# Kernel optimization log

Measured on AMD Instinct MI355X. Metric: run time of the kernel, lower is better.

## Reference

```python
import jax, jax.numpy as jnp
import numpy as np


def dct_matrix(n):
    # orthonormal DCT-II matrix, matches scipy.fftpack.dct(norm='ortho')
    k = jnp.arange(n, dtype=jnp.float32)[:, None]
    i = jnp.arange(n, dtype=jnp.float32)[None, :]
    D = jnp.cos(jnp.pi * (2.0 * i + 1.0) * k / (2.0 * n))
    s = jnp.where(k == 0, jnp.sqrt(1.0 / n), jnp.sqrt(2.0 / n))
    return (D * s).astype(jnp.float32)


def mad_mask(h, w):
    eps = 1e-10
    v1 = int(min(h, w) * 0.1)
    v2 = int(min(h, w) * 0.7)
    v3 = min(h, w)
    xy = jnp.maximum(jnp.arange(h, dtype=jnp.float32)[:, None],
                     jnp.arange(w, dtype=jnp.float32)[None, :])
    m = jnp.where(xy <= v1, 1.0 - xy / (v1 + eps) * 0.95,
        jnp.where(xy <= v2, 0.01,
        jnp.where(xy <= v3, (xy - v2) / (v3 - v2) * 0.3, 0.5)))
    return m.astype(jnp.float32)


def setup_inputs() -> dict:
    key = jax.random.key(0)
    ks = jax.random.split(key, 8)
    num_layers, token_length, C = 24, 100, 1024
    N, B = 1024, 32  # h = w = 32
    patch = 16
    val = np.sqrt(6.0 / float(3 * patch * patch + C))
    feats = jax.random.normal(ks[0], (1 + N, B, C), dtype=jnp.float32)
    learnable_tokens = jax.random.uniform(ks[1], (num_layers, token_length, C),
                                          minval=-val, maxval=val, dtype=jnp.float32)
    lim = 1.0 / np.sqrt(C)
    W_t2f = jax.random.uniform(ks[2], (C, C), minval=-lim, maxval=lim, dtype=jnp.float32)
    b_t2f = jax.random.uniform(ks[3], (C,), minval=-lim, maxval=lim, dtype=jnp.float32)
    W_df = jax.random.uniform(ks[4], (C, C), minval=-lim, maxval=lim, dtype=jnp.float32)
    b_df = jax.random.uniform(ks[5], (C,), minval=-lim, maxval=lim, dtype=jnp.float32)
    return {
        'feats': feats,
        'layer': 5,
        'learnable_tokens': learnable_tokens,
        'scale': jnp.float32(0.001),
        'W_t2f': W_t2f,
        'b_t2f': b_t2f,
        'W_df': W_df,
        'b_df': b_df,
    }


def reference(feats, layer, learnable_tokens, scale, W_t2f, b_t2f, W_df, b_df):
    # has_cls_token=True, batch_first=False (defaults)
    cls_tok, x = feats[:1], feats[1:]          # [1,B,C], [N,B,C]
    N, B, C = x.shape
    h = int(np.sqrt(N)); w = h
    # NOTE: original does a raw reshape (N,B,C) -> (B,C,h,w); replicate faithfully.
    ximg = x.reshape(B, C, h, w)
    # --- MAD_decompose: 2D orthonormal DCT-II per (b, c) image ---
    D = dct_matrix(h)
    feat_dct = jnp.einsum('ik,bckl,jl->bcij', D, ximg, D)
    mask = mad_mask(h, w)                      # [h,w]
    cal = feat_dct * (1.0 - mask)              # high-frequency (causal) part
    cal = cal.reshape(N, B, C)                 # raw reshape as in torch code
    # --- forward_delta_feat ---
    tokens = learnable_tokens[layer]           # [M,C]
    attn = jnp.einsum('nbc,mc->nbm', cal, tokens) * (C ** -0.5)
    attn = jax.nn.softmax(attn, axis=-1)
    t2f = tokens[1:] @ W_t2f.T + b_t2f         # [M-1,C]
    df = jnp.einsum('nbm,mc->nbc', attn[:, :, 1:], t2f)
    df = (df + cal) @ W_df.T + b_df            # [N,B,C]
    # --- MAD_compose_fast: ifft2 approximation of IDCT, clamp to [0,255] ---
    fc = df.reshape(B, C, h, w).astype(jnp.complex64)
    out = jnp.clip(jnp.real(jnp.fft.ifft2(fc, norm='ortho')), 0.0, 255.0)
    out = out.reshape(N, B, C).astype(jnp.float32)
    x = x + out * scale
    return jnp.concatenate([cls_tok, x], axis=0)
```

## Files before the change

kernel.cpp:

```cpp
#include <hip/hip_runtime.h>

typedef unsigned short u16;
typedef u16 ushort8 __attribute__((ext_vector_type(8)));
typedef u16 ushort4v __attribute__((ext_vector_type(4)));
typedef __bf16 bf16x8 __attribute__((ext_vector_type(8)));
typedef float f32x4 __attribute__((ext_vector_type(4)));

#define PI_F 3.14159265358979323846f

__device__ __forceinline__ u16 f2bf(float f) {
  union { float f; unsigned int u; } v; v.f = f;
  unsigned int r = v.u + 0x7fffu + ((v.u >> 16) & 1u);
  return (u16)(r >> 16);
}
__device__ __forceinline__ float bf2f(u16 u) {
  union { unsigned int u; float f; } v; v.u = ((unsigned int)u) << 16;
  return v.f;
}

__device__ __forceinline__ void gload16(const u16* g, u16* l) {
  __builtin_amdgcn_global_load_lds((const __attribute__((address_space(1))) void*)g,
                                   (__attribute__((address_space(3))) void*)l, 16, 0, 0);
}

__device__ __forceinline__ void stage_tile(const u16* __restrict__ G, int ld, int row0, int k0,
                                           u16* lds, int wid, int lane) {
  int seg = wid * 32;
  const u16* gp = G + (size_t)(row0 + seg + (lane >> 2)) * ld + k0 + (lane & 3) * 8;
  gload16(gp, lds + seg * 32);
  gload16(gp + (size_t)16 * ld, lds + (seg + 16) * 32);
}

#define WAIT_VM(N) asm volatile("s_waitcnt vmcnt(" #N ")" ::: "memory")
#define RAW_BARRIER() asm volatile("s_barrier" ::: "memory")

__device__ __forceinline__ float im_val(int r, int c) {
  float xy = (float)(r > c ? r : c);
  float m = (xy <= 3.0f) ? (1.0f - xy * (0.95f / 3.0f))
           : ((xy <= 22.0f) ? 0.01f : ((xy - 22.0f) * 0.03f));
  return 1.0f - m;
}
__device__ __forceinline__ float dct_val(int r, int c) {
  int a = ((2 * c + 1) * r) & 127;
  float s = (r == 0) ? 0.17677669529663687f : 0.25f;
  return cosf((float)a * (PI_F / 64.0f)) * s;
}

__global__ __launch_bounds__(256) void k_prep(const float* __restrict__ feats,
                                              const float* __restrict__ lt, const int* __restrict__ layerp,
                                              const float* __restrict__ Wt2f,
                                              u16* __restrict__ xb, u16* __restrict__ wt_bf,
                                              u16* __restrict__ tok_bf, u16* __restrict__ A2,
                                              float* __restrict__ outp) {
  int tid = blockIdx.x * 256 + threadIdx.x;
  int L = *layerp;
  const float4* in4 = (const float4*)(feats + 32768);
  ushort4v* xb4 = (ushort4v*)xb;
  #pragma unroll
  for (int rep = 0; rep < 16; ++rep) {
    int j = tid + rep * 524288;
    float4 v = in4[j];
    ushort4v o;
    o[0] = f2bf(v.x); o[1] = f2bf(v.y); o[2] = f2bf(v.z); o[3] = f2bf(v.w);
    xb4[j] = o;
  }
  ((ushort8*)A2)[tid] = (ushort8){0,0,0,0,0,0,0,0};
  if (tid < 262144) {
    float4 v = ((const float4*)Wt2f)[tid];
    ushort4v o;
    o[0] = f2bf(v.x); o[1] = f2bf(v.y); o[2] = f2bf(v.z); o[3] = f2bf(v.w);
    ((ushort4v*)wt_bf)[tid] = o;
  }
  if (tid < 32768) {
    outp[tid] = feats[tid];
    int m = tid >> 8;
    ushort4v o = (ushort4v){0,0,0,0};
    if (m < 99) {
      float4 v = *(const float4*)(lt + (size_t)L * 102400 + (size_t)(m + 1) * 1024 + (tid & 255) * 4);
      o[0] = f2bf(v.x); o[1] = f2bf(v.y); o[2] = f2bf(v.z); o[3] = f2bf(v.w);
    }
    ((ushort4v*)tok_bf)[tid] = o;
  }
}

__device__ void mdct_row(const float* __restrict__ row, u16* __restrict__ dst, float* sm, int t) {
  float* Ms = sm; float* T1 = sm + 1056; float* Dsh = sm + 2112;
  for (int i = t; i < 1024; i += 256) {
    int r = i >> 5, c = i & 31;
    Dsh[r * 33 + c] = dct_val(r, c);
    Ms[r * 33 + c] = row[i] * im_val(r, c);
  }
  __syncthreads();
  int k = t >> 3, l0 = (t & 7) * 4;
  float a0 = 0, a1 = 0, a2 = 0, a3 = 0;
  #pragma unroll 8
  for (int i = 0; i < 32; ++i) {
    float d = Dsh[i * 33 + k];
    const float* mr = &Ms[i * 33 + l0];
    a0 += d * mr[0]; a1 += d * mr[1]; a2 += d * mr[2]; a3 += d * mr[3];
  }
  T1[k * 33 + l0 + 0] = a0; T1[k * 33 + l0 + 1] = a1;
  T1[k * 33 + l0 + 2] = a2; T1[k * 33 + l0 + 3] = a3;
  __syncthreads();
  float b0 = 0, b1 = 0, b2 = 0, b3 = 0;
  #pragma unroll 8
  for (int j = 0; j < 32; ++j) {
    float u = T1[k * 33 + j];
    b0 += u * Dsh[j * 33 + l0 + 0];
    b1 += u * Dsh[j * 33 + l0 + 1];
    b2 += u * Dsh[j * 33 + l0 + 2];
    b3 += u * Dsh[j * 33 + l0 + 3];
  }
  ushort4v o;
  o[0] = f2bf(b0); o[1] = f2bf(b1); o[2] = f2bf(b2); o[3] = f2bf(b3);
  *(ushort4v*)(dst + k * 32 + l0) = o;
}

__global__ __launch_bounds__(256) void k_setupA(const float* __restrict__ Wdf, const float* __restrict__ bdf,
                                                const float* __restrict__ lt, const int* __restrict__ layerp,
                                                float* __restrict__ weff_f, u16* __restrict__ weff_bf,
                                                float* __restrict__ beff, u16* __restrict__ tok2) {
  __shared__ __align__(16) float sm[14784];
  int bid = blockIdx.x, t = threadIdx.x;
  if (bid < 256) {
    float* In = sm; float* Uc = sm + 4224; float* Us = sm + 8448;
    float* Csh = sm + 12672; float* Ssh = sm + 13728;
    int c0 = bid * 4;
    for (int i = t; i < 1024; i += 256) {
      int r = i >> 5, c = i & 31;
      float ang = (float)((r * c) & 31) * (PI_F / 16.0f);
      Csh[r * 33 + c] = cosf(ang); Ssh[r * 33 + c] = sinf(ang);
    }
    { int cc = t & 3, v0 = t >> 2;
      for (int v = v0; v < 1024; v += 64)
        In[cc * 1056 + (v >> 5) * 33 + (v & 31)] = Wdf[(size_t)v * 1024 + c0 + cc]; }
    __syncthreads();
    int cc = t >> 6, L2 = t & 63, p = L2 & 31, h = L2 >> 5;
    for (int j = h * 16; j < h * 16 + 16; ++j) {
      float ac = 0, as = 0;
      #pragma unroll 8
      for (int i = 0; i < 32; ++i) {
        float m = In[cc * 1056 + i * 33 + j];
        ac += Csh[p * 33 + i] * m;
        as += Ssh[p * 33 + i] * m;
      }
      Uc[cc * 1056 + p * 33 + j] = ac;
      Us[cc * 1056 + p * 33 + j] = as;
    }
    __syncthreads();
    for (int q = h * 16; q < h * 16 + 16; ++q) {
      float acc = 0;
      #pragma unroll 8
      for (int j = 0; j < 32; ++j)
        acc += Uc[cc * 1056 + p * 33 + j] * Csh[q * 33 + j] -
               Us[cc * 1056 + p * 33 + j] * Ssh[q * 33 + j];
      float val = acc * 0.03125f;
      size_t idx = (size_t)(p * 32 + q) * 1024 + c0 + cc;
      weff_f[idx] = val;
      weff_bf[idx] = f2bf(val);
    }
  } else if (bid == 256) {
    float* Bsh = sm; float* Uc = sm + 1056; float* Us = sm + 2112;
    float* Csh = sm + 3168; float* Ssh = sm + 4224;
    for (int i = t; i < 1024; i += 256) {
      int r = i >> 5, c = i & 31;
      float ang = (float)((r * c) & 31) * (PI_F / 16.0f);
      Csh[r * 33 + c] = cosf(ang); Ssh[r * 33 + c] = sinf(ang);
      Bsh[r * 33 + c] = bdf[i];
    }
    __syncthreads();
    for (int idx = t; idx < 1024; idx += 256) {
      int p = idx >> 5, j = idx & 31;
      float ac = 0, as = 0;
      #pragma unroll 8
      for (int i = 0; i < 32; ++i) {
        float m = Bsh[i * 33 + j];
        ac += Csh[p * 33 + i] * m;
        as += Ssh[p * 33 + i] * m;
      }
      Uc[p * 33 + j] = ac; Us[p * 33 + j] = as;
    }
    __syncthreads();
    for (int idx = t; idx < 1024; idx += 256) {
      int p = idx >> 5, q = idx & 31;
      float acc = 0;
      #pragma unroll 8
      for (int jj = 0; jj < 32; ++jj)
        acc += Uc[p * 33 + jj] * Csh[q * 33 + jj] - Us[p * 33 + jj] * Ssh[q * 33 + jj];
      beff[idx] = acc * 0.03125f;
    }
  } else {
    int p = bid - 257;
    if (p >= 100) {
      *(ushort4v*)(tok2 + (size_t)p * 1024 + t * 4) = (ushort4v){0,0,0,0};
      return;
    }
    mdct_row(lt + (size_t)(*layerp) * 102400 + (size_t)p * 1024, tok2 + (size_t)p * 1024, sm, t);
  }
}

template <int NT>
__device__ __forceinline__ void gemm128_core(const u16* __restrict__ A, int lda,
                                             const u16* __restrict__ B, int ldb,
                                             int g0, int c0, u16* smem,
                                             f32x4 (&acc)[4][4], int wid, int lane) {
  int wr = wid >> 1, wc = wid & 1, cl = lane & 15, rg = lane >> 4;
  stage_tile(A, lda, g0, 0, smem, wid, lane);
  stage_tile(B, ldb, c0, 0, smem + 12288, wid, lane);
  stage_tile(A, lda, g0, 32, smem + 4096, wid, lane);
  stage_tile(B, ldb, c0, 32, smem + 16384, wid, lane);
  int cur = 0;
  #pragma unroll 1
  for (int kt = 0; kt < NT; ++kt) {
    if (kt == NT - 1) { WAIT_VM(0); } else { WAIT_VM(4); }
    RAW_BARRIER();
    if (kt + 2 < NT) {
      int slot = (cur == 0) ? 2 : cur - 1;
      stage_tile(A, lda, g0, (kt + 2) * 32, smem + slot * 4096, wid, lane);
      stage_tile(B, ldb, c0, (kt + 2) * 32, smem + 12288 + slot * 4096, wid, lane);
    }
    const u16* pa = smem + cur * 4096;
    const u16* pb = smem + 12288 + cur * 4096;
    bf16x8 af[4], bv[4];
    #pragma unroll
    for (int mf = 0; mf < 4; mf++)
      af[mf] = *(const bf16x8*)(pa + (wr * 64 + mf * 16 + cl) * 32 + rg * 8);
    #pragma unroll
    for (int nf = 0; nf < 4; nf++)
      bv[nf] = *(const bf16x8*)(pb + (wc * 64 + nf * 16 + cl) * 32 + rg * 8);
    #pragma unroll
    for (int mf = 0; mf < 4; mf++)
      #pragma unroll
      for (int nf = 0; nf < 4; nf++)
        acc[mf][nf] = __builtin_amdgcn_mfma_f32_16x16x32_bf16(af[mf], bv[nf], acc[mf][nf], 0, 0, 0);
    cur = (cur == 2) ? 0 : cur + 1;
  }
}

__global__ __launch_bounds__(256) void k_setupB(const float* __restrict__ weff_f,
                                                const u16* __restrict__ tok_bf, const u16* __restrict__ wt_bf,
                                                const float* __restrict__ bt2f,
                                                u16* __restrict__ w2, u16* __restrict__ t2f) {
  __shared__ __align__(16) u16 smem[24576];
  int bid = blockIdx.x, t = threadIdx.x;
  if (bid < 1024) {
    mdct_row(weff_f + (size_t)bid * 1024, w2 + (size_t)bid * 1024, (float*)smem, t);
  } else {
    int bn = bid - 1024;
    int lane = t & 63, wid = t >> 6;
    int wr = wid >> 1, wc = wid & 1, cl = lane & 15, rg = lane >> 4;
    f32x4 acc[4][4];
    #pragma unroll
    for (int i = 0; i < 4; i++)
      #pragma unroll
      for (int j = 0; j < 4; j++) acc[i][j] = (f32x4){0.f,0.f,0.f,0.f};
    gemm128_core<32>(tok_bf, 1024, wt_bf, 1024, 0, bn * 128, smem, acc, wid, lane);
    #pragma unroll
    for (int mf = 0; mf < 4; mf++)
      #pragma unroll
      for (int nf = 0; nf < 4; nf++) {
        int col = bn * 128 + wc * 64 + nf * 16 + cl;
        #pragma unroll
        for (int r = 0; r < 4; r++) {
          int row = wr * 64 + mf * 16 + rg * 4 + r;
          t2f[(size_t)row * 1024 + col] = (row < 99) ? f2bf(acc[mf][nf][r] + bt2f[col]) : (u16)0;
        }
      }
  }
}

__global__ __launch_bounds__(256) void k_setupC(const u16* __restrict__ weff_bf, const u16* __restrict__ t2f,
                                                const u16* __restrict__ xb, const u16* __restrict__ tok2,
                                                u16* __restrict__ Gt, u16* __restrict__ A2) {
  __shared__ __align__(16) u16 smem[24576];
  int bid = blockIdx.x, t = threadIdx.x;
  int lane = t & 63, wid = t >> 6;
  if (bid < 8) {
    int wr = wid >> 1, wc = wid & 1, cl = lane & 15, rg = lane >> 4;
    f32x4 acc[4][4];
    #pragma unroll
    for (int i = 0; i < 4; i++)
      #pragma unroll
      for (int j = 0; j < 4; j++) acc[i][j] = (f32x4){0.f,0.f,0.f,0.f};
    gemm128_core<32>(weff_bf, 1024, t2f, 1024, bid * 128, 0, smem, acc, wid, lane);
    #pragma unroll
    for (int mf = 0; mf < 4; mf++)
      #pragma unroll
      for (int nf = 0; nf < 4; nf++) {
        int col = wc * 64 + nf * 16 + cl;
        #pragma unroll
        for (int r = 0; r < 4; r++) {
          int row = bid * 128 + wr * 64 + mf * 16 + rg * 4 + r;
          Gt[(size_t)row * 128 + col] = f2bf(acc[mf][nf][r]);
        }
      }
  } else {
    int g0 = (bid - 8) * 128;
    int cl = lane & 15, rg = lane >> 4;
    f32x4 acc[2][7];
    #pragma unroll
    for (int i = 0; i < 2; i++)
      #pragma unroll
      for (int j = 0; j < 7; j++) acc[i][j] = (f32x4){0.f,0.f,0.f,0.f};
    stage_tile(xb, 1024, g0, 0, smem, wid, lane);
    stage_tile(tok2, 1024, 0, 0, smem + 12288, wid, lane);
    stage_tile(xb, 1024, g0, 32, smem + 4096, wid, lane);
    stage_tile(tok2, 1024, 0, 32, smem + 16384, wid, lane);
    int cur = 0;
    #pragma unroll 1
    for (int kt = 0; kt < 32; ++kt) {
      if (kt == 31) { WAIT_VM(0); } else { WAIT_VM(4); }
      RAW_BARRIER();
      if (kt + 2 < 32) {
        int slot = (cur == 0) ? 2 : cur - 1;
        stage_tile(xb, 1024, g0, (kt + 2) * 32, smem + slot * 4096, wid, lane);
        stage_tile(tok2, 1024, 0, (kt + 2) * 32, smem + 12288 + slot * 4096, wid, lane);
      }
      const u16* pa = smem + cur * 4096;
      const u16* pb = smem + 12288 + cur * 4096;
      bf16x8 a0 = *(const bf16x8*)(pa + (wid * 32 + cl) * 32 + rg * 8);
      bf16x8 a1 = *(const bf16x8*)(pa + (wid * 32 + 16 + cl) * 32 + rg * 8);
      #pragma unroll
      for (int nf = 0; nf < 7; nf++) {
        bf16x8 bv = *(const bf16x8*)(pb + (nf * 16 + cl) * 32 + rg * 8);
        acc[0][nf] = __builtin_amdgcn_mfma_f32_16x16x32_bf16(a0, bv, acc[0][nf], 0, 0, 0);
        acc[1][nf] = __builtin_amdgcn_mfma_f32_16x16x32_bf16(a1, bv, acc[1][nf], 0, 0, 0);
      }
      cur = (cur == 2) ? 0 : cur + 1;
    }
    #pragma unroll
    for (int mf = 0; mf < 2; mf++) {
      #pragma unroll
      for (int r = 0; r < 4; r++) {
        int grow = g0 + wid * 32 + mf * 16 + rg * 4 + r;
        float v[7];
        float mx = -1e30f;
        #pragma unroll
        for (int nf = 0; nf < 7; nf++) {
          int m = nf * 16 + cl;
          v[nf] = acc[mf][nf][r] * 0.03125f;
          if (m < 100) mx = fmaxf(mx, v[nf]);
        }
        #pragma unroll
        for (int d = 1; d < 16; d <<= 1) mx = fmaxf(mx, __shfl_xor(mx, d));
        float s = 0;
        #pragma unroll
        for (int nf = 0; nf < 7; nf++) {
          int m = nf * 16 + cl;
          float e = (m < 100) ? __expf(v[nf] - mx) : 0.0f;
          v[nf] = e; s += e;
        }
        #pragma unroll
        for (int d = 1; d < 16; d <<= 1) s += __shfl_xor(s, d);
        float inv = 1.0f / s;
        #pragma unroll
        for (int nf = 0; nf < 7; nf++) {
          int m = nf * 16 + cl;
          if (m >= 1 && m < 100) A2[(size_t)grow * 128 + (m - 1)] = f2bf(v[nf] * inv);
        }
      }
    }
  }
}

__global__ __launch_bounds__(256) void k_main(const u16* __restrict__ xb, const u16* __restrict__ w2,
                                              const u16* __restrict__ a2, const u16* __restrict__ gt,
                                              const float* __restrict__ beff, const float* __restrict__ feats,
                                              const float* __restrict__ scalep, float* __restrict__ outf) {
  __shared__ __align__(16) u16 smem[24576];
  int t = threadIdx.x, lane = t & 63, wid = t >> 6;
  int bid = blockIdx.x;
  int xcd = bid & 7, local = bid >> 3;
  int super = local >> 5, within = local & 31;
  int bm = xcd * 32 + super * 4 + (within & 3);
  int bn = within >> 2;
  int g0 = bm * 128, c0 = bn * 128;
  int wr = wid >> 1, wc = wid & 1;
  int cl = lane & 15, rg = lane >> 4;
  f32x4 acc[4][4];
  #pragma unroll
  for (int i = 0; i < 4; i++)
    #pragma unroll
    for (int j = 0; j < 4; j++) acc[i][j] = (f32x4){0.f,0.f,0.f,0.f};

  auto stage = [&](int kt, int slot) {
    u16* sa = smem + slot * 4096;
    u16* sb = smem + 12288 + slot * 4096;
    if (kt < 32) {
      stage_tile(xb, 1024, g0, kt * 32, sa, wid, lane);
      stage_tile(w2, 1024, c0, kt * 32, sb, wid, lane);
    } else {
      int k0 = (kt - 32) * 32;
      stage_tile(a2, 128, g0, k0, sa, wid, lane);
      stage_tile(gt, 128, c0, k0, sb, wid, lane);
    }
  };

  stage(0, 0);
  stage(1, 1);
  int cur = 0;
  #pragma unroll 1
  for (int kt = 0; kt < 36; ++kt) {
    if (kt == 35) { WAIT_VM(0); } else { WAIT_VM(4); }
    RAW_BARRIER();
    if (kt + 2 < 36) stage(kt + 2, (cur == 0) ? 2 : cur - 1);
    const u16* pa = smem + cur * 4096;
    const u16* pb = smem + 12288 + cur * 4096;
    bf16x8 af[4], bv[4];
    #pragma unroll
    for (int mf = 0; mf < 4; mf++)
      af[mf] = *(const bf16x8*)(pa + (wr * 64 + mf * 16 + cl) * 32 + rg * 8);
    #pragma unroll
    for (int nf = 0; nf < 4; nf++)
      bv[nf] = *(const bf16x8*)(pb + (wc * 64 + nf * 16 + cl) * 32 + rg * 8);
    #pragma unroll
    for (int mf = 0; mf < 4; mf++)
      #pragma unroll
      for (int nf = 0; nf < 4; nf++)
        acc[mf][nf] = __builtin_amdgcn_mfma_f32_16x16x32_bf16(af[mf], bv[nf], acc[mf][nf], 0, 0, 0);
    cur = (cur == 2) ? 0 : cur + 1;
  }

  float sc = *scalep;
  #pragma unroll
  for (int mf = 0; mf < 4; mf++) {
    #pragma unroll
    for (int nf = 0; nf < 4; nf++) {
      int col = c0 + wc * 64 + nf * 16 + cl;
      #pragma unroll
      for (int r = 0; r < 4; r++) {
        int row = g0 + wr * 64 + mf * 16 + rg * 4 + r;
        size_t idx = (size_t)row * 1024 + col;
        float val = acc[mf][nf][r] + beff[col];
        float rr = fminf(fmaxf(val, 0.f), 255.f);
        outf[32768 + idx] = feats[32768 + idx] + rr * sc;
      }
    }
  }
}

extern "C" void kernel_launch(void* const* d_in, const int* in_sizes, int n_in,
                              void* d_out, int out_size, void* d_ws, size_t ws_size,
                              hipStream_t stream) {
  const float* feats  = (const float*)d_in[0];
  const int*   layerp = (const int*)d_in[1];
  const float* lt     = (const float*)d_in[2];
  const float* scalep = (const float*)d_in[3];
  const float* Wt2f   = (const float*)d_in[4];
  const float* bt2f   = (const float*)d_in[5];
  const float* Wdf    = (const float*)d_in[6];
  const float* bdf    = (const float*)d_in[7];
  float* outp = (float*)d_out;

  char* ws = (char*)d_ws;
  float* beff   = (float*)(ws + 0);
  float* weff_f = (float*)(ws + 65536);
  u16* weff_bf = (u16*)(ws + 4259840);
  u16* w2      = (u16*)(ws + 6356992);
  u16* tok_bf  = (u16*)(ws + 8454144);
  u16* wt_bf   = (u16*)(ws + 8716288);
  u16* tok2    = (u16*)(ws + 10813440);
  u16* t2f     = (u16*)(ws + 11075584);
  u16* Gt      = (u16*)(ws + 11337728);
  u16* A2      = (u16*)(ws + 11599872);
  u16* xb      = (u16*)(ws + 19988480);

  k_prep<<<2048, 256, 0, stream>>>(feats, lt, layerp, Wt2f, xb, wt_bf, tok_bf, A2, outp);
  k_setupA<<<385, 256, 0, stream>>>(Wdf, bdf, lt, layerp, weff_f, weff_bf, beff, tok2);
  k_setupB<<<1032, 256, 0, stream>>>(weff_f, tok_bf, wt_bf, bt2f, w2, t2f);
  k_setupC<<<264, 256, 0, stream>>>(weff_bf, t2f, xb, tok2, Gt, A2);
  k_main<<<2048, 256, 0, stream>>>(xb, w2, A2, Gt, beff, feats, scalep, outp);
}
```

Measured before the change: 246.8 us.

## Enlarge main GEMM tile to 256x256 with swizzled LDS and split-K staging

The main fused GEMM kernel moves from 128x128 tiles with 4 waves to 256x256 tiles with 8 waves per block, each wave owning a 128x64 output patch. LDS staging now uses an XOR swizzle to avoid bank conflicts, and a 64-wide K step is split into two 32-wide halves with separate barriers so loads for upcoming halves overlap with compute. MFMA issue priority is raised around the matrix-multiply bursts. The larger tile cuts global and L2 traffic per FLOP, at the cost of 128KB LDS per block and higher register pressure, and the grid drops to 512 blocks.

```diff
diff --git a/kernel.cpp b/kernel.cpp
--- a/kernel.cpp
+++ b/kernel.cpp
@@ -32,6 +32,7 @@
 }
 
 #define WAIT_VM(N) asm volatile("s_waitcnt vmcnt(" #N ")" ::: "memory")
+#define WAIT_LGKM0() asm volatile("s_waitcnt lgkmcnt(0)" ::: "memory")
 #define RAW_BARRIER() asm volatile("s_barrier" ::: "memory")
 
 __device__ __forceinline__ float im_val(int r, int c) {
@@ -363,77 +364,106 @@
   }
 }
 
-__global__ __launch_bounds__(256) void k_main(const u16* __restrict__ xb, const u16* __restrict__ w2,
-                                              const u16* __restrict__ a2, const u16* __restrict__ gt,
-                                              const float* __restrict__ beff, const float* __restrict__ feats,
-                                              const float* __restrict__ scalep, float* __restrict__ outf) {
-  __shared__ __align__(16) u16 smem[24576];
-  int t = threadIdx.x, lane = t & 63, wid = t >> 6;
+__global__ __launch_bounds__(512, 2) void k_main(const u16* __restrict__ xb, const u16* __restrict__ w2,
+                                                 const u16* __restrict__ a2, const u16* __restrict__ gt,
+                                                 const float* __restrict__ beff, const float* __restrict__ feats,
+                                                 const float* __restrict__ scalep, float* __restrict__ outf) {
+  __shared__ __align__(16) u16 smem[65536];
+  int tid = threadIdx.x, lane = tid & 63, wid = tid >> 6;
+  int wr = wid >> 2, wc = wid & 3;
+  int cl = lane & 15, rg = lane >> 4;
   int bid = blockIdx.x;
-  int xcd = bid & 7, local = bid >> 3;
-  int super = local >> 5, within = local & 31;
-  int bm = xcd * 32 + super * 4 + (within & 3);
-  int bn = within >> 2;
-  int g0 = bm * 128, c0 = bn * 128;
-  int wr = wid >> 1, wc = wid & 1;
-  int cl = lane & 15, rg = lane >> 4;
-  f32x4 acc[4][4];
+  int swz = (bid & 7) * 64 + (bid >> 3);
+  int bm = swz >> 2, bn = swz & 3;
+  int g0 = bm * 256, c0 = bn * 256;
+
+  f32x4 acc[8][4];
   #pragma unroll
-  for (int i = 0; i < 4; i++)
+  for (int i = 0; i < 8; i++)
     #pragma unroll
     for (int j = 0; j < 4; j++) acc[i][j] = (f32x4){0.f,0.f,0.f,0.f};
 
-  auto stage = [&](int kt, int slot) {
-    u16* sa = smem + slot * 4096;
-    u16* sb = smem + 12288 + slot * 4096;
-    if (kt < 32) {
-      stage_tile(xb, 1024, g0, kt * 32, sa, wid, lane);
-      stage_tile(w2, 1024, c0, kt * 32, sb, wid, lane);
+  auto stage_region = [&](const u16* G, int ld, int row0, int k0, u16* reg) {
+    #pragma unroll
+    for (int l = 0; l < 2; ++l) {
+      int r_loc = (l * 8 + wid) * 16 + (lane >> 2);
+      int cB = ((lane & 3) << 4) ^ (((r_loc >> 1) & 3) << 4);
+      gload16(G + (size_t)(row0 + r_loc) * ld + k0 + (cB >> 1), reg + (l * 8 + wid) * 512);
+    }
+  };
+  auto stage = [&](int t, int kh) {
+    int par = t & 1;
+    u16* RA = smem + (size_t)(kh * 2 + par) * 8192;
+    u16* RB = smem + 32768 + (size_t)(kh * 2 + par) * 8192;
+    if (t < 16) {
+      stage_region(xb, 1024, g0, t * 64 + kh * 32, RA);
+      stage_region(w2, 1024, c0, t * 64 + kh * 32, RB);
     } else {
-      int k0 = (kt - 32) * 32;
-      stage_tile(a2, 128, g0, k0, sa, wid, lane);
-      stage_tile(gt, 128, c0, k0, sb, wid, lane);
+      int k0 = (t - 16) * 64 + kh * 32;
+      stage_region(a2, 128, g0, k0, RA);
+      stage_region(gt, 128, c0, k0, RB);
     }
   };
-
+  auto frag = [&](const u16* R, int row) -> bf16x8 {
+    int off = row * 32 + ((rg * 8) ^ (((row >> 1) & 3) << 3));
+    return *(const bf16x8*)(R + off);
+  };
+  auto compute_half = [&](int kh, int par) {
+    const u16* RA = smem + (size_t)(kh * 2 + par) * 8192;
+    const u16* RB = smem + 32768 + (size_t)(kh * 2 + par) * 8192;
+    bf16x8 bv[4];
+    #pragma unroll
+    for (int nf = 0; nf < 4; nf++) bv[nf] = frag(RB, wc * 64 + nf * 16 + cl);
+    #pragma unroll
+    for (int mg = 0; mg < 2; mg++) {
+      bf16x8 af[4];
+      #pragma unroll
+      for (int mf = 0; mf < 4; mf++) af[mf] = frag(RA, wr * 128 + mg * 64 + mf * 16 + cl);
+      __builtin_amdgcn_s_setprio(1);
+      #pragma unroll
+      for (int mf = 0; mf < 4; mf++)
+        #pragma unroll
+        for (int nf = 0; nf < 4; nf++)
+          acc[mg * 4 + mf][nf] = __builtin_amdgcn_mfma_f32_16x16x32_bf16(af[mf], bv[nf], acc[mg * 4 + mf][nf], 0, 0, 0);
+      __builtin_amdgcn_s_setprio(0);
+    }
+  };
+
+  const int NT = 18;
   stage(0, 0);
-  stage(1, 1);
-  int cur = 0;
+  stage(0, 1);
+  stage(1, 0);
   #pragma unroll 1
-  for (int kt = 0; kt < 36; ++kt) {
-    if (kt == 35) { WAIT_VM(0); } else { WAIT_VM(4); }
+  for (int t = 0; t < NT; ++t) {
+    int par = t & 1;
+    WAIT_LGKM0();
+    if (t == NT - 1) { WAIT_VM(4); } else { WAIT_VM(8); }
     RAW_BARRIER();
-    if (kt + 2 < 36) stage(kt + 2, (cur == 0) ? 2 : cur - 1);
-    const u16* pa = smem + cur * 4096;
-    const u16* pb = smem + 12288 + cur * 4096;
-    bf16x8 af[4], bv[4];
-    #pragma unroll
-    for (int mf = 0; mf < 4; mf++)
-      af[mf] = *(const bf16x8*)(pa + (wr * 64 + mf * 16 + cl) * 32 + rg * 8);
-    #pragma unroll
-    for (int nf = 0; nf < 4; nf++)
-      bv[nf] = *(const bf16x8*)(pb + (wc * 64 + nf * 16 + cl) * 32 + rg * 8);
-    #pragma unroll
-    for (int mf = 0; mf < 4; mf++)
-      #pragma unroll
-      for (int nf = 0; nf < 4; nf++)
-        acc[mf][nf] = __builtin_amdgcn_mfma_f32_16x16x32_bf16(af[mf], bv[nf], acc[mf][nf], 0, 0, 0);
-    cur = (cur == 2) ? 0 : cur + 1;
+    if (t + 1 < NT) stage(t + 1, 1);
+    compute_half(0, par);
+    WAIT_LGKM0();
+    if (t == NT - 1) { WAIT_VM(0); } else { WAIT_VM(8); }
+    RAW_BARRIER();
+    if (t + 2 < NT) stage(t + 2, 0);
+    compute_half(1, par);
   }
 
   float sc = *scalep;
   #pragma unroll
-  for (int mf = 0; mf < 4; mf++) {
-    #pragma unroll
-    for (int nf = 0; nf < 4; nf++) {
-      int col = c0 + wc * 64 + nf * 16 + cl;
-      #pragma unroll
-      for (int r = 0; r < 4; r++) {
-        int row = g0 + wr * 64 + mf * 16 + rg * 4 + r;
-        size_t idx = (size_t)row * 1024 + col;
-        float val = acc[mf][nf][r] + beff[col];
-        float rr = fminf(fmaxf(val, 0.f), 255.f);
-        outf[32768 + idx] = feats[32768 + idx] + rr * sc;
+  for (int mg = 0; mg < 2; mg++) {
+    #pragma unroll
+    for (int mf = 0; mf < 4; mf++) {
+      #pragma unroll
+      for (int nf = 0; nf < 4; nf++) {
+        int col = c0 + wc * 64 + nf * 16 + cl;
+        #pragma unroll
+        for (int r = 0; r < 4; r++) {
+          int row = g0 + wr * 128 + mg * 64 + mf * 16 + rg * 4 + r;
+          size_t idx = (size_t)row * 1024 + col;
+          float val = acc[mg * 4 + mf][nf][r] + beff[col];
+          float rr = fminf(fmaxf(val, 0.f), 255.f);
+          outf[32768 + idx] = feats[32768 + idx] + rr * sc;
+        }
       }
     }
   }
@@ -469,5 +499,5 @@
   k_setupA<<<385, 256, 0, stream>>>(Wdf, bdf, lt, layerp, weff_f, weff_bf, beff, tok2);
   k_setupB<<<1032, 256, 0, stream>>>(weff_f, tok_bf, wt_bf, bt2f, w2, t2f);
   k_setupC<<<264, 256, 0, stream>>>(weff_bf, t2f, xb, tok2, Gt, A2);
-  k_main<<<2048, 256, 0, stream>>>(xb, w2, A2, Gt, beff, feats, scalep, outp);
-}
+  k_main<<<512, 512, 0, stream>>>(xb, w2, A2, Gt, beff, feats, scalep, outp);
+}
```

Result: slower. 257.8 us (+4.5%).
